# Kernel tuning notes

Hardware: AMD Instinct MI355X
Metric: run time of the kernel (lower is better)

## Reference

```python
import jax, jax.numpy as jnp
import numpy as np


def _butter_bandpass_ba(N, w1, w2):
    """Digital Butterworth bandpass design (scipy.signal.iirfilter equivalent),
    fs = 2 half-cycles/sample, output='ba'. Done in float64 numpy at setup time."""
    # analog lowpass prototype (buttap): no zeros, N poles on unit circle, k=1
    p = -np.exp(1j * np.pi * np.arange(-N + 1, N, 2) / (2.0 * N))
    k = 1.0
    fs = 2.0
    warped = 2.0 * fs * np.tan(np.pi * np.array([w1, w2]) / fs)
    bw = warped[1] - warped[0]
    wo = np.sqrt(warped[0] * warped[1])
    # lp2bp_zpk
    p_lp = p * bw / 2.0
    sq = np.sqrt(p_lp ** 2 - wo ** 2)
    p_bp = np.concatenate([p_lp + sq, p_lp - sq])          # 2N poles
    z_bp = np.zeros(N, dtype=complex)                       # N zeros at origin
    k_bp = k * bw ** N
    # bilinear_zpk with fs=2
    fs2 = 2.0 * fs
    z_d = (fs2 + z_bp) / (fs2 - z_bp)
    p_d = (fs2 + p_bp) / (fs2 - p_bp)
    z_d = np.concatenate([z_d, -np.ones(len(p_bp) - len(z_bp))])
    k_d = k_bp * np.real(np.prod(fs2 - z_bp) / np.prod(fs2 - p_bp))
    b = np.real(k_d * np.poly(z_d))
    a = np.real(np.poly(p_d))
    return b, a


def setup_inputs() -> dict:
    key = jax.random.key(0)
    B, T = 512, 65536
    x = jax.random.normal(key, (B, T), dtype=jnp.float32)
    b_np, a_np = _butter_bandpass_ba(4, 0.1, 0.4)           # len 9 each
    return {
        "x": x,
        "b": jnp.asarray(b_np, dtype=jnp.float32),
        "a": jnp.asarray(a_np, dtype=jnp.float32),
    }


def _lfilter(x, b, a):
    """Direct-form II transposed IIR filter with zero initial state.
    x: (B, T); b, a: (M,). Equivalent to torchaudio lfilter (clamp=False)."""
    b = b / a[0]
    a = a / a[0]
    b0 = b[0]
    bt = b[1:]          # (M-1,)
    at = a[1:]          # (M-1,)

    def step(z, xt):
        # z: (B, M-1) delay state, xt: (B,)
        y = b0 * xt + z[:, 0]
        z_new = xt[:, None] * bt[None, :] - y[:, None] * at[None, :]
        z_new = z_new.at[:, :-1].add(z[:, 1:])
        return z_new, y

    z0 = jnp.zeros((x.shape[0], b.shape[0] - 1), dtype=x.dtype)
    _, y = jax.lax.scan(step, z0, x.T)                      # y: (T, B)
    return y.T


def reference(x, b, a):
    # filtfilt: forward pass, then filter the time-reversed result and reverse back
    y = _lfilter(x, b, a)
    y = _lfilter(y[:, ::-1], b, a)[:, ::-1]
    return y
```

## Files before the change

kernel.cpp:

```cpp
#include <hip/hip_runtime.h>

constexpr int BLOCK  = 64;
constexpr int NS     = 128;
constexpr int WARM   = 64;
constexpr int CF     = 68;
constexpr int CB     = 64;
constexpr int TILE   = NS * CB;
constexpr int RF     = NS * CF;
constexpr int WARM_Q = WARM / 4;
constexpr int QF     = CF / 4;
constexpr int QB     = CB / 4;
constexpr int XQ     = (WARM + RF) / 4;
constexpr int LSZ    = (XQ - 1) + ((XQ - 1) >> 3) + 1;
constexpr int TILE_Q = TILE / 4;
constexpr int SITER  = (XQ + BLOCK - 1) / BLOCK;

typedef float v2 __attribute__((ext_vector_type(2)));

__device__ __forceinline__ int lam(int g) { return g + (g >> 3); }

__device__ __forceinline__ unsigned pkbf(float a, float b) {
    unsigned r;
    asm("v_cvt_pk_bf16_f32 %0, %1, %2" : "=v"(r) : "v"(a), "v"(b));
    return r;
}
__device__ __forceinline__ float lo16(unsigned u) { return __uint_as_float(u << 16); }
__device__ __forceinline__ float hi16(unsigned u) { return __uint_as_float(u & 0xFFFF0000u); }

__device__ __forceinline__ v2 fma2(v2 a, v2 b, v2 c) {
#if defined(__has_builtin) && __has_builtin(__builtin_elementwise_fma)
    return __builtin_elementwise_fma(a, b, c);
#else
    return v2{fmaf(a.x, b.x, c.x), fmaf(a.y, b.y, c.y)};
#endif
}

__global__ __launch_bounds__(BLOCK, 2) void iir_fused(
    const float* __restrict__ x, float* __restrict__ y,
    const float* __restrict__ bc, const float* __restrict__ ac,
    int T, int tilesPerRow)
{
    __shared__ uint2 lds[LSZ];

    const int tid     = threadIdx.x;
    const int row     = blockIdx.x / tilesPerRow;
    const int tileIdx = blockIdx.x - row * tilesPerRow;
    const int t0      = tileIdx * TILE;

    const float* __restrict__ xr = x + (size_t)row * T;
    float* __restrict__       yr = y + (size_t)row * T;

#pragma unroll 7
    for (int it = 0; it < SITER; ++it) {
        const int g = it * BLOCK + tid;
        if (g < XQ) {
            const int t = t0 - WARM + 4 * g;
            const float4 v = (t < 0 || t >= T) ? float4{0.f, 0.f, 0.f, 0.f}
                                               : *(const float4*)(xr + t);
            lds[lam(g)] = uint2{pkbf(v.x, v.y), pkbf(v.z, v.w)};
        }
    }

    const float inv = 1.0f / ac[0];
    const v2 b02 = {bc[0] * inv, bc[0] * inv};
    v2 bt2[8], nat2[8];
#pragma unroll
    for (int i = 0; i < 8; ++i) {
        const float bi = bc[i + 1] * inv;
        const float ai = -(ac[i + 1] * inv);
        bt2[i]  = v2{bi, bi};
        nat2[i] = v2{ai, ai};
    }

    v2 z2[8];
    auto step2 = [&](v2 xv) -> v2 {
        const v2 yv = fma2(b02, xv, z2[0]);
#pragma unroll
        for (int i = 0; i < 7; ++i)
            z2[i] = fma2(nat2[i], yv, fma2(bt2[i], xv, z2[i + 1]));
        z2[7] = fma2(nat2[7], yv, bt2[7] * xv);
        return yv;
    };

    __syncthreads();

    const int sA = tid, sB = tid + BLOCK;

#pragma unroll
    for (int i = 0; i < 8; ++i) z2[i] = v2{0.f, 0.f};

#pragma unroll
    for (int i = 0; i < WARM_Q; ++i) {
        const uint2 qA = lds[lam(17 * sA + i)];
        const uint2 qB = lds[lam(17 * sB + i)];
        step2(v2{lo16(qA.x), lo16(qB.x)}); step2(v2{hi16(qA.x), hi16(qB.x)});
        step2(v2{lo16(qA.y), lo16(qB.y)}); step2(v2{hi16(qA.y), hi16(qB.y)});
    }

    __syncthreads();

    const int vlim = T - t0;
#pragma unroll
    for (int j = 0; j < QF; ++j) {
        const int ia = lam(17 * sA + WARM_Q + j);
        const int ib = lam(17 * sB + WARM_Q + j);
        const uint2 qA = lds[ia];
        const uint2 qB = lds[ib];
        const v2 o0 = step2(v2{lo16(qA.x), lo16(qB.x)});
        const v2 o1 = step2(v2{hi16(qA.x), hi16(qB.x)});
        const v2 o2 = step2(v2{lo16(qA.y), lo16(qB.y)});
        const v2 o3 = step2(v2{hi16(qA.y), hi16(qB.y)});
        const int va = CF * sA + 4 * j, vb = CF * sB + 4 * j;
        const float a0 = (va + 0 < vlim) ? o0.x : 0.f;
        const float a1 = (va + 1 < vlim) ? o1.x : 0.f;
        const float a2 = (va + 2 < vlim) ? o2.x : 0.f;
        const float a3 = (va + 3 < vlim) ? o3.x : 0.f;
        const float b0v = (vb + 0 < vlim) ? o0.y : 0.f;
        const float b1v = (vb + 1 < vlim) ? o1.y : 0.f;
        const float b2v = (vb + 2 < vlim) ? o2.y : 0.f;
        const float b3v = (vb + 3 < vlim) ? o3.y : 0.f;
        lds[ia] = uint2{pkbf(a0, a1), pkbf(a2, a3)};
        lds[ib] = uint2{pkbf(b0v, b1v), pkbf(b2v, b3v)};
    }

    __syncthreads();

#pragma unroll
    for (int i = 0; i < 8; ++i) z2[i] = v2{0.f, 0.f};

#pragma unroll
    for (int i = 0; i < WARM_Q; ++i) {
        const uint2 qA = lds[lam(WARM_Q + 16 * sA + 31 - i)];
        const uint2 qB = lds[lam(WARM_Q + 16 * sB + 31 - i)];
        step2(v2{hi16(qA.y), hi16(qB.y)}); step2(v2{lo16(qA.y), lo16(qB.y)});
        step2(v2{hi16(qA.x), hi16(qB.x)}); step2(v2{lo16(qA.x), lo16(qB.x)});
    }

    __syncthreads();

#pragma unroll
    for (int j = 0; j < QB; ++j) {
        const int ia = lam(WARM_Q + 16 * sA + 15 - j);
        const int ib = lam(WARM_Q + 16 * sB + 15 - j);
        const uint2 qA = lds[ia];
        const uint2 qB = lds[ib];
        const v2 o0 = step2(v2{hi16(qA.y), hi16(qB.y)});
        const v2 o1 = step2(v2{lo16(qA.y), lo16(qB.y)});
        const v2 o2 = step2(v2{hi16(qA.x), hi16(qB.x)});
        const v2 o3 = step2(v2{lo16(qA.x), lo16(qB.x)});
        lds[ia] = uint2{pkbf(o3.x, o2.x), pkbf(o1.x, o0.x)};
        lds[ib] = uint2{pkbf(o3.y, o2.y), pkbf(o1.y, o0.y)};
    }

    __syncthreads();

#pragma unroll 8
    for (int it = 0; it < TILE_Q / BLOCK; ++it) {
        const int q = it * BLOCK + tid;
        const uint2 u = lds[lam(WARM_Q + q)];
        const float4 o = {lo16(u.x), hi16(u.x), lo16(u.y), hi16(u.y)};
        *(float4*)(yr + t0 + 4 * q) = o;
    }
}

extern "C" void kernel_launch(void* const* d_in, const int* in_sizes, int n_in,
                              void* d_out, int out_size, void* d_ws, size_t ws_size,
                              hipStream_t stream)
{
    const float* x = (const float*)d_in[0];
    const float* b = (const float*)d_in[1];
    const float* a = (const float*)d_in[2];
    float* out = (float*)d_out;

    const int T = 65536;
    const int B = in_sizes[0] / T;
    const int tilesPerRow = T / TILE;
    const int totalBlocks = B * tilesPerRow;

    dim3 block(BLOCK);
    dim3 grid(totalBlocks);

    iir_fused<<<grid, block, 0, stream>>>(x, out, b, a, T, tilesPerRow);
}
```

Measured before the change: 291.7 us.

## Process two tiles per block with register prefetch of the next tile

Result: slower. 432.6 us (+48.3%).

```diff
diff --git a/kernel.cpp b/kernel.cpp
--- a/kernel.cpp
+++ b/kernel.cpp
@@ -14,6 +14,7 @@
 constexpr int LSZ    = (XQ - 1) + ((XQ - 1) >> 3) + 1;
 constexpr int TILE_Q = TILE / 4;
 constexpr int SITER  = (XQ + BLOCK - 1) / BLOCK;
+constexpr int NITER  = 2;
 
 typedef float v2 __attribute__((ext_vector_type(2)));
 
@@ -26,6 +27,8 @@
 }
 __device__ __forceinline__ float lo16(unsigned u) { return __uint_as_float(u << 16); }
 __device__ __forceinline__ float hi16(unsigned u) { return __uint_as_float(u & 0xFFFF0000u); }
+
+#define WSYNC() asm volatile("s_waitcnt lgkmcnt(0)" ::: "memory")
 
 __device__ __forceinline__ v2 fma2(v2 a, v2 b, v2 c) {
 #if defined(__has_builtin) && __has_builtin(__builtin_elementwise_fma)
@@ -42,24 +45,8 @@
 {
     __shared__ uint2 lds[LSZ];
 
-    const int tid     = threadIdx.x;
-    const int row     = blockIdx.x / tilesPerRow;
-    const int tileIdx = blockIdx.x - row * tilesPerRow;
-    const int t0      = tileIdx * TILE;
-
-    const float* __restrict__ xr = x + (size_t)row * T;
-    float* __restrict__       yr = y + (size_t)row * T;
-
-#pragma unroll 7
-    for (int it = 0; it < SITER; ++it) {
-        const int g = it * BLOCK + tid;
-        if (g < XQ) {
-            const int t = t0 - WARM + 4 * g;
-            const float4 v = (t < 0 || t >= T) ? float4{0.f, 0.f, 0.f, 0.f}
-                                               : *(const float4*)(xr + t);
-            lds[lam(g)] = uint2{pkbf(v.x, v.y), pkbf(v.z, v.w)};
-        }
-    }
+    const int tid      = threadIdx.x;
+    const int tileBase = blockIdx.x * NITER;
 
     const float inv = 1.0f / ac[0];
     const v2 b02 = {bc[0] * inv, bc[0] * inv};
@@ -82,84 +69,125 @@
         return yv;
     };
 
-    __syncthreads();
+    float4 vr[SITER];
+
+    auto load_tile = [&](int tg) {
+        const int row = tg / tilesPerRow;
+        const int t0  = (tg - row * tilesPerRow) * TILE;
+        const float* __restrict__ xr = x + (size_t)row * T;
+#pragma unroll
+        for (int it = 0; it < SITER; ++it) {
+            const int g = it * BLOCK + tid;
+            if (g < XQ) {
+                const int t = t0 - WARM + 4 * g;
+                vr[it] = (t < 0 || t >= T) ? float4{0.f, 0.f, 0.f, 0.f}
+                                           : *(const float4*)(xr + t);
+            }
+        }
+    };
+    auto write_tile = [&]() {
+#pragma unroll
+        for (int it = 0; it < SITER; ++it) {
+            const int g = it * BLOCK + tid;
+            if (g < XQ)
+                lds[lam(g)] = uint2{pkbf(vr[it].x, vr[it].y),
+                                    pkbf(vr[it].z, vr[it].w)};
+        }
+    };
+
+    load_tile(tileBase);
+    write_tile();
+    WSYNC();
 
     const int sA = tid, sB = tid + BLOCK;
 
-#pragma unroll
-    for (int i = 0; i < 8; ++i) z2[i] = v2{0.f, 0.f};
-
-#pragma unroll
-    for (int i = 0; i < WARM_Q; ++i) {
-        const uint2 qA = lds[lam(17 * sA + i)];
-        const uint2 qB = lds[lam(17 * sB + i)];
-        step2(v2{lo16(qA.x), lo16(qB.x)}); step2(v2{hi16(qA.x), hi16(qB.x)});
-        step2(v2{lo16(qA.y), lo16(qB.y)}); step2(v2{hi16(qA.y), hi16(qB.y)});
-    }
-
-    __syncthreads();
-
-    const int vlim = T - t0;
-#pragma unroll
-    for (int j = 0; j < QF; ++j) {
-        const int ia = lam(17 * sA + WARM_Q + j);
-        const int ib = lam(17 * sB + WARM_Q + j);
-        const uint2 qA = lds[ia];
-        const uint2 qB = lds[ib];
-        const v2 o0 = step2(v2{lo16(qA.x), lo16(qB.x)});
-        const v2 o1 = step2(v2{hi16(qA.x), hi16(qB.x)});
-        const v2 o2 = step2(v2{lo16(qA.y), lo16(qB.y)});
-        const v2 o3 = step2(v2{hi16(qA.y), hi16(qB.y)});
-        const int va = CF * sA + 4 * j, vb = CF * sB + 4 * j;
-        const float a0 = (va + 0 < vlim) ? o0.x : 0.f;
-        const float a1 = (va + 1 < vlim) ? o1.x : 0.f;
-        const float a2 = (va + 2 < vlim) ? o2.x : 0.f;
-        const float a3 = (va + 3 < vlim) ? o3.x : 0.f;
-        const float b0v = (vb + 0 < vlim) ? o0.y : 0.f;
-        const float b1v = (vb + 1 < vlim) ? o1.y : 0.f;
-        const float b2v = (vb + 2 < vlim) ? o2.y : 0.f;
-        const float b3v = (vb + 3 < vlim) ? o3.y : 0.f;
-        lds[ia] = uint2{pkbf(a0, a1), pkbf(a2, a3)};
-        lds[ib] = uint2{pkbf(b0v, b1v), pkbf(b2v, b3v)};
-    }
-
-    __syncthreads();
-
-#pragma unroll
-    for (int i = 0; i < 8; ++i) z2[i] = v2{0.f, 0.f};
-
-#pragma unroll
-    for (int i = 0; i < WARM_Q; ++i) {
-        const uint2 qA = lds[lam(WARM_Q + 16 * sA + 31 - i)];
-        const uint2 qB = lds[lam(WARM_Q + 16 * sB + 31 - i)];
-        step2(v2{hi16(qA.y), hi16(qB.y)}); step2(v2{lo16(qA.y), lo16(qB.y)});
-        step2(v2{hi16(qA.x), hi16(qB.x)}); step2(v2{lo16(qA.x), lo16(qB.x)});
-    }
-
-    __syncthreads();
-
-#pragma unroll
-    for (int j = 0; j < QB; ++j) {
-        const int ia = lam(WARM_Q + 16 * sA + 15 - j);
-        const int ib = lam(WARM_Q + 16 * sB + 15 - j);
-        const uint2 qA = lds[ia];
-        const uint2 qB = lds[ib];
-        const v2 o0 = step2(v2{hi16(qA.y), hi16(qB.y)});
-        const v2 o1 = step2(v2{lo16(qA.y), lo16(qB.y)});
-        const v2 o2 = step2(v2{hi16(qA.x), hi16(qB.x)});
-        const v2 o3 = step2(v2{lo16(qA.x), lo16(qB.x)});
-        lds[ia] = uint2{pkbf(o3.x, o2.x), pkbf(o1.x, o0.x)};
-        lds[ib] = uint2{pkbf(o3.y, o2.y), pkbf(o1.y, o0.y)};
-    }
-
-    __syncthreads();
+    for (int k = 0; k < NITER; ++k) {
+        const int tg  = tileBase + k;
+        const int row = tg / tilesPerRow;
+        const int t0  = (tg - row * tilesPerRow) * TILE;
+        float* __restrict__ yr = y + (size_t)row * T;
+
+        if (k + 1 < NITER) load_tile(tg + 1);
+
+#pragma unroll
+        for (int i = 0; i < 8; ++i) z2[i] = v2{0.f, 0.f};
+
+#pragma unroll
+        for (int i = 0; i < WARM_Q; ++i) {
+            const uint2 qA = lds[lam(17 * sA + i)];
+            const uint2 qB = lds[lam(17 * sB + i)];
+            step2(v2{lo16(qA.x), lo16(qB.x)}); step2(v2{hi16(qA.x), hi16(qB.x)});
+            step2(v2{lo16(qA.y), lo16(qB.y)}); step2(v2{hi16(qA.y), hi16(qB.y)});
+        }
+
+        WSYNC();
+
+        const int vlim = T - t0;
+#pragma unroll
+        for (int j = 0; j < QF; ++j) {
+            const int ia = lam(17 * sA + WARM_Q + j);
+            const int ib = lam(17 * sB + WARM_Q + j);
+            const uint2 qA = lds[ia];
+            const uint2 qB = lds[ib];
+            const v2 o0 = step2(v2{lo16(qA.x), lo16(qB.x)});
+            const v2 o1 = step2(v2{hi16(qA.x), hi16(qB.x)});
+            const v2 o2 = step2(v2{lo16(qA.y), lo16(qB.y)});
+            const v2 o3 = step2(v2{hi16(qA.y), hi16(qB.y)});
+            const int va = CF * sA + 4 * j, vb = CF * sB + 4 * j;
+            const float a0 = (va + 0 < vlim) ? o0.x : 0.f;
+            const float a1 = (va + 1 < vlim) ? o1.x : 0.f;
+            const float a2 = (va + 2 < vlim) ? o2.x : 0.f;
+            const float a3 = (va + 3 < vlim) ? o3.x : 0.f;
+            const float b0v = (vb + 0 < vlim) ? o0.y : 0.f;
+            const float b1v = (vb + 1 < vlim) ? o1.y : 0.f;
+            const float b2v = (vb + 2 < vlim) ? o2.y : 0.f;
+            const float b3v = (vb + 3 < vlim) ? o3.y : 0.f;
+            lds[ia] = uint2{pkbf(a0, a1), pkbf(a2, a3)};
+            lds[ib] = uint2{pkbf(b0v, b1v), pkbf(b2v, b3v)};
+        }
+
+        WSYNC();
+
+#pragma unroll
+        for (int i = 0; i < 8; ++i) z2[i] = v2{0.f, 0.f};
+
+#pragma unroll
+        for (int i = 0; i < WARM_Q; ++i) {
+            const uint2 qA = lds[lam(WARM_Q + 16 * sA + 31 - i)];
+            const uint2 qB = lds[lam(WARM_Q + 16 * sB + 31 - i)];
+            step2(v2{hi16(qA.y), hi16(qB.y)}); step2(v2{lo16(qA.y), lo16(qB.y)});
+            step2(v2{hi16(qA.x), hi16(qB.x)}); step2(v2{lo16(qA.x), lo16(qB.x)});
+        }
+
+        WSYNC();
+
+#pragma unroll
+        for (int j = 0; j < QB; ++j) {
+            const int ia = lam(WARM_Q + 16 * sA + 15 - j);
+            const int ib = lam(WARM_Q + 16 * sB + 15 - j);
+            const uint2 qA = lds[ia];
+            const uint2 qB = lds[ib];
+            const v2 o0 = step2(v2{hi16(qA.y), hi16(qB.y)});
+            const v2 o1 = step2(v2{lo16(qA.y), lo16(qB.y)});
+            const v2 o2 = step2(v2{hi16(qA.x), hi16(qB.x)});
+            const v2 o3 = step2(v2{lo16(qA.x), lo16(qB.x)});
+            lds[ia] = uint2{pkbf(o3.x, o2.x), pkbf(o1.x, o0.x)};
+            lds[ib] = uint2{pkbf(o3.y, o2.y), pkbf(o1.y, o0.y)};
+        }
+
+        WSYNC();
 
 #pragma unroll 8
-    for (int it = 0; it < TILE_Q / BLOCK; ++it) {
-        const int q = it * BLOCK + tid;
-        const uint2 u = lds[lam(WARM_Q + q)];
-        const float4 o = {lo16(u.x), hi16(u.x), lo16(u.y), hi16(u.y)};
-        *(float4*)(yr + t0 + 4 * q) = o;
+        for (int it = 0; it < TILE_Q / BLOCK; ++it) {
+            const int q = it * BLOCK + tid;
+            const uint2 u = lds[lam(WARM_Q + q)];
+            const float4 o = {lo16(u.x), hi16(u.x), lo16(u.y), hi16(u.y)};
+            *(float4*)(yr + t0 + 4 * q) = o;
+        }
+
+        if (k + 1 < NITER) write_tile();
+
+        WSYNC();
     }
 }
 
@@ -175,10 +203,9 @@
     const int T = 65536;
     const int B = in_sizes[0] / T;
     const int tilesPerRow = T / TILE;
-    const int totalBlocks = B * tilesPerRow;
+    const int totalTiles  = B * tilesPerRow;
+    const int grid        = totalTiles / NITER;
 
     dim3 block(BLOCK);
-    dim3 grid(totalBlocks);
-
     iir_fused<<<grid, block, 0, stream>>>(x, out, b, a, T, tilesPerRow);
 }
```
